# Kernel optimization log

Measured on AMD Instinct MI355X. Metric: run time of the kernel, lower is better.

The kernel has to match this reference:

```python
import jax, jax.numpy as jnp
import numpy as np

EPS = 1e-4  # performer softmax-kernel stabilizer
LN_EPS = 1e-5


def _layernorm(x, g, b):
    m = jnp.mean(x, axis=-1, keepdims=True)
    v = jnp.mean(jnp.square(x - m), axis=-1, keepdims=True)
    return (x - m) * jax.lax.rsqrt(v + LN_EPS) * g + b


def _softmax_features(x, proj, is_query):
    # FAVOR+ positive softmax-kernel features. x: [B,H,N,Dh], proj: [M,Dh]
    d = x.shape[-1]
    xn = x * (d ** -0.25)                      # data normalizer d^{-1/4}
    u = jnp.einsum('bhnd,md->bhnm', xn, proj)  # [B,H,N,M]
    diag = 0.5 * jnp.sum(jnp.square(xn), axis=-1, keepdims=True)
    if is_query:
        stab = jnp.max(u, axis=-1, keepdims=True)
    else:
        stab = jnp.max(u, axis=(-2, -1), keepdims=True)
    ratio = proj.shape[0] ** -0.5
    return ratio * (jnp.exp(u - diag - stab) + EPS)


def reference(x, proj, ln1_g, ln1_b, ln2_g, ln2_b, W1, b1, W2, b2):
    B, N, E = x.shape
    M, Dh = proj.shape
    H = E // Dh

    # --- multi-head fast attention sublayer (pre-LN, q=k=v, no dropout) ---
    h = _layernorm(x, ln1_g, ln1_b)
    qkv = h.reshape(B, N, H, Dh).transpose(0, 2, 1, 3)     # [B,H,N,Dh]
    q_p = _softmax_features(qkv, proj, is_query=True)      # [B,H,N,M]
    k_p = _softmax_features(qkv, proj, is_query=False)     # [B,H,N,M]

    # non-causal linear attention: O(N*M*Dh)
    k_sum = jnp.sum(k_p, axis=-2)                          # [B,H,M]
    d_inv = 1.0 / jnp.einsum('bhnm,bhm->bhn', q_p, k_sum)  # [B,H,N]
    ctx = jnp.einsum('bhnm,bhnd->bhmd', k_p, qkv)          # [B,H,M,Dh]
    attn = jnp.einsum('bhnm,bhmd,bhn->bhnd', q_p, ctx, d_inv)
    attn = attn.transpose(0, 2, 1, 3).reshape(B, N, E)
    x = x + attn

    # --- MLP sublayer (pre-LN, GELU, dropout off in eval) ---
    h2 = _layernorm(x, ln2_g, ln2_b)
    h2 = jax.nn.gelu(h2 @ W1 + b1, approximate=False) @ W2 + b2
    return x + h2


def setup_inputs() -> dict:
    B, N, E, H, M, F = 4, 2048, 768, 12, 256, 3072
    Dh = E // H
    key = jax.random.key(0)
    ks = jax.random.split(key, 4)
    return {
        'x': jax.random.normal(ks[0], (B, N, E), jnp.float32),
        'proj': jax.random.normal(ks[1], (M, Dh), jnp.float32),
        'ln1_g': jnp.ones((E,), jnp.float32),
        'ln1_b': jnp.zeros((E,), jnp.float32),
        'ln2_g': jnp.ones((E,), jnp.float32),
        'ln2_b': jnp.zeros((E,), jnp.float32),
        'W1': jax.random.normal(ks[2], (E, F), jnp.float32) * 0.02,
        'b1': jnp.zeros((F,), jnp.float32),
        'W2': jax.random.normal(ks[3], (F, E), jnp.float32) * 0.02,
        'b2': jnp.zeros((E,), jnp.float32),
    }
```

## Files before the change

kernel.cpp:

```cpp
#include <hip/hip_runtime.h>
#include <hip/hip_bf16.h>
#include <math.h>

#define B_    4
#define N_    2048
#define E_    768
#define H_    12
#define M_    256
#define F_    3072
#define DH_   64
#define BN_   (B_ * N_)
#define BH_   (B_ * H_)
#define NSP_  16

#define EPS_F     1e-4f
#define LN_EPS_F  1e-5f
#define DNORM_F   0.35355339059327373f
#define DIAGC_F   0.0625f

typedef __attribute__((ext_vector_type(8))) short bf16x8;
typedef __attribute__((ext_vector_type(4))) float f32x4;

static __device__ __forceinline__ float to_f32(float v) { return v; }
static __device__ __forceinline__ float to_f32(__hip_bfloat16 v) { return __bfloat162float(v); }
static __device__ __forceinline__ short f2bf(float v) {
    __hip_bfloat16 b = __float2bfloat16(v);
    return *reinterpret_cast<short*>(&b);
}

static __device__ __forceinline__ float fast_gelu(float x) {
    float xc = fminf(fmaxf(x, -9.f), 9.f);
    float y = 0.7978845608028654f * (xc + 0.044715f * xc * xc * xc);
    float tt = __expf(-2.f * y);
    return x * __builtin_amdgcn_rcpf(1.f + tt);
}

static __device__ __forceinline__ void gld_lds16(const void* g, void* lds) {
    __builtin_amdgcn_global_load_lds((const __attribute__((address_space(1))) void*)g,
                                     (__attribute__((address_space(3))) void*)lds, 16, 0, 0);
}

__global__ void probe_kernel(const unsigned int* __restrict__ g1, int* __restrict__ flag) {
    if (threadIdx.x == 0 && blockIdx.x == 0)
        *flag = (*g1 == 0x3F803F80u) ? 1 : 0;
}

__global__ void convert_kernel(const void* __restrict__ src, __hip_bfloat16* __restrict__ dst,
                               int n, const int* __restrict__ flag) {
    int isb = *flag;
    int i = blockIdx.x * blockDim.x + threadIdx.x;
    int stride = gridDim.x * blockDim.x;
    if (isb) {
        const unsigned short* s = (const unsigned short*)src;
        unsigned short* d = (unsigned short*)dst;
        for (; i < n; i += stride) d[i] = s[i];
    } else {
        const float* s = (const float*)src;
        for (; i < n; i += stride) dst[i] = __float2bfloat16(s[i]);
    }
}

__global__ void convert_transpose_kernel(const void* __restrict__ src,
                                         __hip_bfloat16* __restrict__ dst,
                                         int R, int C, const int* __restrict__ flag) {
    __shared__ __hip_bfloat16 tile[32][33];
    int isb = *flag;
    int c0 = blockIdx.x * 32, r0 = blockIdx.y * 32;
    int tx = threadIdx.x & 31, ty = threadIdx.x >> 5;
    if (isb) {
        const unsigned short* s = (const unsigned short*)src;
        for (int j = 0; j < 4; ++j) {
            int r = ty + j * 8;
            ((unsigned short*)&tile[r][tx])[0] = s[(size_t)(r0 + r) * C + c0 + tx];
        }
    } else {
        const float* s = (const float*)src;
        for (int j = 0; j < 4; ++j) {
            int r = ty + j * 8;
            tile[r][tx] = __float2bfloat16(s[(size_t)(r0 + r) * C + c0 + tx]);
        }
    }
    __syncthreads();
    for (int j = 0; j < 4; ++j) {
        int r = ty + j * 8;
        dst[(size_t)(c0 + r) * R + r0 + tx] = tile[tx][r];
    }
}

template <typename TIn>
__global__ void ln_kernel(const TIn* __restrict__ x,
                          const __hip_bfloat16* __restrict__ g,
                          const __hip_bfloat16* __restrict__ b,
                          __hip_bfloat16* __restrict__ hout,
                          float* __restrict__ diag ) {
    int row = blockIdx.x;
    int t = threadIdx.x;
    __shared__ float rs[256], rq[256];
    __shared__ float hrow[E_];

    float xv[3];
    const TIn* xr = x + (size_t)row * E_;
    float s = 0.f, q = 0.f;
    for (int i = 0; i < 3; ++i) {
        xv[i] = to_f32(xr[t + i * 256]);
        s += xv[i];
        q += xv[i] * xv[i];
    }
    rs[t] = s; rq[t] = q;
    __syncthreads();
    for (int off = 128; off > 0; off >>= 1) {
        if (t < off) { rs[t] += rs[t + off]; rq[t] += rq[t + off]; }
        __syncthreads();
    }
    float mean = rs[0] * (1.0f / E_);
    float var  = rq[0] * (1.0f / E_) - mean * mean;
    float rinv = rsqrtf(fmaxf(var, 0.0f) + LN_EPS_F);

    __hip_bfloat16* hr = hout + (size_t)row * E_;
    for (int i = 0; i < 3; ++i) {
        int e = t + i * 256;
        float hv = (xv[i] - mean) * rinv * __bfloat162float(g[e]) + __bfloat162float(b[e]);
        hr[e] = __float2bfloat16(hv);
        hrow[e] = hv;
    }
    if (diag != nullptr) {
        __syncthreads();
        if (t < H_) {
            float acc = 0.f;
            for (int k = 0; k < DH_; ++k) { float v = hrow[t * DH_ + k]; acc += v * v; }
            diag[row * H_ + t] = DIAGC_F * acc;
        }
    }
}

__global__ __launch_bounds__(256) void ctx_mfma_kernel(
        const __hip_bfloat16* __restrict__ h,
        const __hip_bfloat16* __restrict__ proj,
        const float* __restrict__ diag,
        float* __restrict__ pctx, float* __restrict__ pksum,
        float* __restrict__ pmax, float* __restrict__ pvsum) {
    int sp = blockIdx.x, bh = blockIdx.y;
    int bb = bh / H_, hh = bh % H_;
    int n0 = sp * 128;
    int t = threadIdx.x, lane = t & 63, w = t >> 6;
    int lm = lane & 15, kg = lane >> 4;

    __shared__ __align__(16) short hv_s[128 * 72];
    __shared__ __align__(16) short vt_s[64 * 136];
    __shared__ __align__(16) short p_s[64 * 72];
    __shared__ __align__(16) short kpt_s[64 * 136];
    __shared__ float ksp_s[4][64];
    __shared__ float dg_s[128];
    __shared__ float wmax_s[4];
    __shared__ float vp_s[4][64];

    for (int it = 0; it < 4; ++it) {
        int c = t + it * 256; int n = c >> 3, kb = c & 7;
        uint4 vld = *(const uint4*)&h[((size_t)(bb * N_ + n0 + n)) * E_ + hh * DH_ + kb * 8];
        *(uint4*)&hv_s[n * 72 + kb * 8] = vld;
        union { uint4 u4; short sh[8]; } uu; uu.u4 = vld;
        for (int j = 0; j < 8; ++j) vt_s[(kb * 8 + j) * 136 + n] = uu.sh[j];
    }
    if (t < 128) dg_s[t] = diag[(size_t)(bb * N_ + n0 + t) * H_ + hh];
    __syncthreads();

    {
        int d = t & 63, rg = t >> 6;
        float s = 0.f;
        for (int n = rg * 32; n < rg * 32 + 32; ++n)
            s += __bfloat162float(*(const __hip_bfloat16*)&hv_s[n * 72 + d]);
        vp_s[rg][d] = s;
    }
    __syncthreads();
    if (t < 64)
        pvsum[((size_t)sp * BH_ + bh) * 64 + t] =
            vp_s[0][t] + vp_s[1][t] + vp_s[2][t] + vp_s[3][t];

    for (int q = 0; q < 4; ++q) {
        __syncthreads();
        for (int it = 0; it < 2; ++it) {
            int c = t + it * 256; int m = c >> 3, kb = c & 7;
            *(uint4*)&p_s[m * 72 + kb * 8] = *(const uint4*)&proj[(size_t)(q * 64 + m) * DH_ + kb * 8];
        }
        __syncthreads();

        f32x4 u[2][4];
        for (int i = 0; i < 2; ++i) for (int j = 0; j < 4; ++j) u[i][j] = (f32x4){0.f,0.f,0.f,0.f};
        for (int kc = 0; kc < 2; ++kc) {
            bf16x8 af[2], bf[4];
            for (int i = 0; i < 2; ++i)
                af[i] = *(const bf16x8*)&hv_s[(w * 32 + i * 16 + lm) * 72 + kc * 32 + kg * 8];
            for (int j = 0; j < 4; ++j)
                bf[j] = *(const bf16x8*)&p_s[(j * 16 + lm) * 72 + kc * 32 + kg * 8];
            for (int i = 0; i < 2; ++i)
                for (int j = 0; j < 4; ++j)
                    u[i][j] = __builtin_amdgcn_mfma_f32_16x16x32_bf16(af[i], bf[j], u[i][j], 0, 0, 0);
        }
        float lmax = -1e30f;
        for (int i = 0; i < 2; ++i) for (int j = 0; j < 4; ++j) for (int r = 0; r < 4; ++r) {
            u[i][j][r] *= DNORM_F;
            lmax = fmaxf(lmax, u[i][j][r]);
        }
        for (int off = 32; off >= 1; off >>= 1) lmax = fmaxf(lmax, __shfl_xor(lmax, off));
        if (lane == 0) wmax_s[w] = lmax;
        __syncthreads();
        float Lmax = fmaxf(fmaxf(wmax_s[0], wmax_s[1]), fmaxf(wmax_s[2], wmax_s[3]));

        float kpart[4] = {0.f, 0.f, 0.f, 0.f};
        for (int i = 0; i < 2; ++i) {
            float dgv[4];
            for (int r = 0; r < 4; ++r) dgv[r] = dg_s[w * 32 + i * 16 + kg * 4 + r];
            for (int j = 0; j < 4; ++j)
                for (int r = 0; r < 4; ++r) {
                    float val = expf(u[i][j][r] - dgv[r] - Lmax);
                    kpart[j] += val;
                    kpt_s[(j * 16 + lm) * 136 + (w * 32 + i * 16 + kg * 4 + r)] = f2bf(val);
                }
        }
        for (int j = 0; j < 4; ++j) {
            kpart[j] += __shfl_xor(kpart[j], 16);
            kpart[j] += __shfl_xor(kpart[j], 32);
        }
        if (lane < 16)
            for (int j = 0; j < 4; ++j) ksp_s[w][j * 16 + lm] = kpart[j];
        __syncthreads();

        f32x4 c4[4];
        for (int jd = 0; jd < 4; ++jd) c4[jd] = (f32x4){0.f,0.f,0.f,0.f};
        for (int kc = 0; kc < 4; ++kc) {
            bf16x8 a = *(const bf16x8*)&kpt_s[(w * 16 + lm) * 136 + kc * 32 + kg * 8];
            for (int jd = 0; jd < 4; ++jd) {
                bf16x8 b = *(const bf16x8*)&vt_s[(jd * 16 + lm) * 136 + kc * 32 + kg * 8];
                c4[jd] = __builtin_amdgcn_mfma_f32_16x16x32_bf16(a, b, c4[jd], 0, 0, 0);
            }
        }
        size_t base = ((size_t)sp * BH_ + bh) * M_ + q * 64 + w * 16;
        for (int jd = 0; jd < 4; ++jd)
            for (int r = 0; r < 4; ++r)
                pctx[(base + kg * 4 + r) * DH_ + jd * 16 + lm] = c4[jd][r];
        if (t < 64)
            pksum[((size_t)sp * BH_ + bh) * M_ + q * 64 + t] =
                ksp_s[0][t] + ksp_s[1][t] + ksp_s[2][t] + ksp_s[3][t];
        if (t == 0) pmax[bh * 64 + sp * 4 + q] = Lmax;
    }
}

__global__ void ctx_reduce_kernel(const float* __restrict__ pctx,
                                  const float* __restrict__ pksum,
                                  const float* __restrict__ pmax,
                                  const float* __restrict__ pvsum,
                                  __hip_bfloat16* __restrict__ ctx_t,
                                  float* __restrict__ ksum) {
    int mb = blockIdx.x, bh = blockIdx.y;
    int t = threadIdx.x;
    __shared__ float hm_s;
    __shared__ float sc_s[16];
    __shared__ float vs_s[64];
    __shared__ float tr_s[64 * 65];
    if (t < 64) {
        float v = pmax[bh * 64 + t];
        for (int off = 32; off >= 1; off >>= 1) v = fmaxf(v, __shfl_xor(v, off));
        if (t == 0) hm_s = v;
        float s = 0.f;
        for (int sp = 0; sp < 16; ++sp) s += pvsum[((size_t)sp * BH_ + bh) * 64 + t];
        vs_s[t] = s;
    }
    __syncthreads();
    if (t < 16) sc_s[t] = expf(pmax[bh * 64 + t * 4 + mb] - hm_s);
    __syncthreads();
    float scl[16];
    for (int sp = 0; sp < 16; ++sp) scl[sp] = sc_s[sp];
    int d = t & 63;
    for (int it = 0; it < 16; ++it) {
        int ml = (t >> 6) + it * 4;
        float acc = 0.f;
        for (int sp = 0; sp < 16; ++sp)
            acc += scl[sp] * pctx[(((size_t)sp * BH_ + bh) * M_ + mb * 64 + ml) * DH_ + d];
        tr_s[ml * 65 + d] = acc + EPS_F * vs_s[d];
    }
    if (t < 64) {
        float ka = 0.f;
        for (int sp = 0; sp < 16; ++sp)
            ka += scl[sp] * pksum[((size_t)sp * BH_ + bh) * M_ + mb * 64 + t];
        ksum[bh * M_ + mb * 64 + t] = ka + EPS_F * (float)N_;
    }
    __syncthreads();
    int mcol = t & 63;
    for (int jt = 0; jt < 16; ++jt) {
        int dl = (t >> 6) + jt * 4;
        ctx_t[((size_t)bh * DH_ + dl) * M_ + mb * 64 + mcol] = __float2bfloat16(tr_s[mcol * 65 + dl]);
    }
}

__global__ void sums_kernel(const __hip_bfloat16* __restrict__ ctx_t,
                            const float* __restrict__ ksum,
                            float* __restrict__ ctxsum, float* __restrict__ kssum) {
    int bh = blockIdx.x, t = threadIdx.x;
    __shared__ float red[256];
    int d = t >> 2, part = t & 3;
    float s = 0.f;
    for (int mm = part * 64; mm < part * 64 + 64; ++mm)
        s += __bfloat162float(ctx_t[((size_t)bh * DH_ + d) * M_ + mm]);
    red[t] = s;
    __syncthreads();
    if (t < 64) ctxsum[bh * 64 + t] = red[t * 4] + red[t * 4 + 1] + red[t * 4 + 2] + red[t * 4 + 3];
    __syncthreads();
    red[t] = ksum[bh * M_ + t];
    __syncthreads();
    for (int off = 128; off > 0; off >>= 1) {
        if (t < off) red[t] += red[t + off];
        __syncthreads();
    }
    if (t == 0) kssum[bh] = red[0];
}

__global__ __launch_bounds__(256) void attn_mfma_kernel(
        const __hip_bfloat16* __restrict__ h,
        const __hip_bfloat16* __restrict__ proj,
        const float* __restrict__ diag,
        const __hip_bfloat16* __restrict__ ctx_t,
        const float* __restrict__ ksum,
        const float* __restrict__ ctxsum,
        const float* __restrict__ kssum,
        const __hip_bfloat16* __restrict__ xin,
        float* __restrict__ x2) {
    int ntile = blockIdx.x, bh = blockIdx.y;
    int bb = bh / H_, hh = bh % H_;
    int n0 = ntile * 128;
    int t = threadIdx.x, lane = t & 63, w = t >> 6;
    int lm = lane & 15, kg = lane >> 4;

    __shared__ __align__(16) short hq_s[128 * 72];
    __shared__ __align__(16) short p_s[64 * 72];
    __shared__ __align__(16) short ct_s[64 * 72];
    __shared__ __align__(16) short qp_s[128 * 72];
    __shared__ float ksum_s[256];
    __shared__ float dg_s[128];
    __shared__ float cs_s[64];
    __shared__ float kss_s;

    for (int it = 0; it < 4; ++it) {
        int c = t + it * 256; int n = c >> 3, kb = c & 7;
        *(uint4*)&hq_s[n * 72 + kb * 8] =
            *(const uint4*)&h[((size_t)(bb * N_ + n0 + n)) * E_ + hh * DH_ + kb * 8];
    }
    if (t < 128) dg_s[t] = diag[(size_t)(bb * N_ + n0 + t) * H_ + hh];
    ksum_s[t] = ksum[bh * M_ + t];
    if (t < 64) cs_s[t] = ctxsum[bh * 64 + t];
    if (t == 0) kss_s = kssum[bh];

    f32x4 o[2][4];
    float qs[2][4], mrun[2][4];
    for (int i = 0; i < 2; ++i)
        for (int jd = 0; jd < 4; ++jd) o[i][jd] = (f32x4){0.f,0.f,0.f,0.f};
    for (int i = 0; i < 2; ++i)
        for (int r = 0; r < 4; ++r) { qs[i][r] = 0.f; mrun[i][r] = -1e30f; }

    for (int mc = 0; mc < 4; ++mc) {
        __syncthreads();
        for (int it = 0; it < 2; ++it) {
            int c = t + it * 256; int m = c >> 3, kb = c & 7;
            *(uint4*)&p_s[m * 72 + kb * 8] = *(const uint4*)&proj[(size_t)(mc * 64 + m) * DH_ + kb * 8];
            *(uint4*)&ct_s[m * 72 + kb * 8] =
                *(const uint4*)&ctx_t[((size_t)bh * DH_ + m) * M_ + mc * 64 + kb * 8];
        }
        __syncthreads();

        f32x4 u[2][4];
        for (int i = 0; i < 2; ++i) for (int j = 0; j < 4; ++j) u[i][j] = (f32x4){0.f,0.f,0.f,0.f};
        for (int kc = 0; kc < 2; ++kc) {
            bf16x8 af[2], bf[4];
            for (int i = 0; i < 2; ++i)
                af[i] = *(const bf16x8*)&hq_s[(w * 32 + i * 16 + lm) * 72 + kc * 32 + kg * 8];
            for (int j = 0; j < 4; ++j)
                bf[j] = *(const bf16x8*)&p_s[(j * 16 + lm) * 72 + kc * 32 + kg * 8];
            for (int i = 0; i < 2; ++i)
                for (int j = 0; j < 4; ++j)
                    u[i][j] = __builtin_amdgcn_mfma_f32_16x16x32_bf16(af[i], bf[j], u[i][j], 0, 0, 0);
        }
        for (int i = 0; i < 2; ++i) for (int j = 0; j < 4; ++j)
            for (int r = 0; r < 4; ++r) u[i][j][r] *= DNORM_F;

        for (int i = 0; i < 2; ++i)
            for (int r = 0; r < 4; ++r) {
                float cm = fmaxf(fmaxf(u[i][0][r], u[i][1][r]), fmaxf(u[i][2][r], u[i][3][r]));
                for (int off = 8; off >= 1; off >>= 1) cm = fmaxf(cm, __shfl_xor(cm, off));
                float mnew = fmaxf(mrun[i][r], cm);
                float sc = expf(mrun[i][r] - mnew);
                mrun[i][r] = mnew;
                qs[i][r] *= sc;
                for (int jd = 0; jd < 4; ++jd) o[i][jd][r] *= sc;
            }
        for (int i = 0; i < 2; ++i) {
            float dgv[4];
            for (int r = 0; r < 4; ++r) dgv[r] = dg_s[w * 32 + i * 16 + kg * 4 + r];
            for (int j = 0; j < 4; ++j) {
                float ksv = ksum_s[mc * 64 + j * 16 + lm];
                for (int r = 0; r < 4; ++r) {
                    float val = expf(u[i][j][r] - dgv[r] - mrun[i][r]);
                    qs[i][r] += val * ksv;
                    qp_s[(w * 32 + i * 16 + kg * 4 + r) * 72 + j * 16 + lm] = f2bf(val);
                }
            }
        }
        __syncthreads();
        for (int kc = 0; kc < 2; ++kc) {
            bf16x8 af[2], bf[4];
            for (int i = 0; i < 2; ++i)
                af[i] = *(const bf16x8*)&qp_s[(w * 32 + i * 16 + lm) * 72 + kc * 32 + kg * 8];
            for (int jd = 0; jd < 4; ++jd)
                bf[jd] = *(const bf16x8*)&ct_s[(jd * 16 + lm) * 72 + kc * 32 + kg * 8];
            for (int i = 0; i < 2; ++i)
                for (int jd = 0; jd < 4; ++jd)
                    o[i][jd] = __builtin_amdgcn_mfma_f32_16x16x32_bf16(af[i], bf[jd], o[i][jd], 0, 0, 0);
        }
    }

    for (int i = 0; i < 2; ++i)
        for (int r = 0; r < 4; ++r)
            for (int off = 8; off >= 1; off >>= 1) qs[i][r] += __shfl_xor(qs[i][r], off);
    float kss = kss_s;
    for (int i = 0; i < 2; ++i)
        for (int r = 0; r < 4; ++r) {
            float dinv = 1.0f / (qs[i][r] + EPS_F * kss);
            size_t row = (size_t)(bb * N_ + n0 + w * 32 + i * 16 + kg * 4 + r);
            for (int jd = 0; jd < 4; ++jd) {
                int dcol = jd * 16 + lm;
                float outv = (o[i][jd][r] + EPS_F * cs_s[dcol]) * dinv;
                int col = hh * DH_ + dcol;
                x2[row * E_ + col] = __bfloat162float(xin[row * E_ + col]) + outv;
            }
        }
}

template <int KK, int NCOLS, int TM, bool DO_GELU>
__global__ __launch_bounds__(256) void mfma_mlp_kernel(
        const __hip_bfloat16* __restrict__ A,
        const __hip_bfloat16* __restrict__ Bt,
        const __hip_bfloat16* __restrict__ bias,
        const float* __restrict__ resid,
        void* __restrict__ outv,
        const int* __restrict__ oflag) {
    constexpr int TN = 128;
    constexpr int WR = TM / 64;
    constexpr int WC = 4 / WR;
    constexpr int PW = TN / WC;
    constexpr int NB = PW / 16;
    constexpr int CA = TM / 16;
    constexpr int CB = TN / 16;
    constexpr int CPS = CA + CB;
    constexpr int CPW = CPS / 4;
    constexpr int LBUF = CPS * 512;
    constexpr int NT = KK / 32;
    constexpr int NXB = NCOLS / TN;
    constexpr int NWG = NXB * (BN_ / TM);
    constexpr int CPX = NWG / 8;

    const int t = threadIdx.x;
    const int bid0 = blockIdx.y * NXB + blockIdx.x;
    const int bid = (bid0 & 7) * CPX + (bid0 >> 3);
    const int col0 = (bid % NXB) * TN;
    const int row0 = (bid / NXB) * TM;

    const int lane = t & 63, w = t >> 6;
    const int wr = w % WR, wc = w / WR;
    const int lm = lane & 15, kg = lane >> 4;
    const int lp = lane ^ ((lane >> 3) & 7);
    const int lr = lp >> 2, lc = (lp & 3) * 8;
    const int sxa = (lm >> 1) << 3;

    __shared__ __align__(16) short Ls[3 * LBUF];

    const __hip_bfloat16* gp[CPW];
    int lof[CPW];
#pragma unroll
    for (int cc = 0; cc < CPW; ++cc) {
        int c = w + cc * 4;
        gp[cc] = (c < CA) ? &A[(size_t)(row0 + c * 16 + lr) * KK + lc]
                          : &Bt[(size_t)(col0 + (c - CA) * 16 + lr) * KK + lc];
        lof[cc] = c * 512;
    }

    f32x4 acc[4][NB];
#pragma unroll
    for (int i = 0; i < 4; ++i)
#pragma unroll
        for (int j = 0; j < NB; ++j)
            acc[i][j] = (f32x4){0.f, 0.f, 0.f, 0.f};

#pragma unroll
    for (int cc = 0; cc < CPW; ++cc) gld_lds16(gp[cc], &Ls[lof[cc]]);
#pragma unroll
    for (int cc = 0; cc < CPW; ++cc) gld_lds16(gp[cc] + 32, &Ls[LBUF + lof[cc]]);

    int cur = 0;
    for (int ts = 0; ts < NT; ++ts) {
        if (ts + 2 < NT) {
            const int nb3 = (cur >= 1) ? (cur - 1) : 2;
            const int ko = (ts + 2) * 32;
#pragma unroll
            for (int cc = 0; cc < CPW; ++cc)
                gld_lds16(gp[cc] + ko, &Ls[nb3 * LBUF + lof[cc]]);
        }
        if (ts + 2 < NT)      asm volatile("s_waitcnt vmcnt(%0)" :: "n"(2 * CPW) : "memory");
        else if (ts + 1 < NT) asm volatile("s_waitcnt vmcnt(%0)" :: "n"(CPW) : "memory");
        else                  asm volatile("s_waitcnt vmcnt(0)" ::: "memory");
        __builtin_amdgcn_s_barrier();

        const short* base = &Ls[cur * LBUF];
        bf16x8 af[4], bfr[NB];
#pragma unroll
        for (int i = 0; i < 4; ++i)
            af[i] = *(const bf16x8*)&base[(((wr * 64 + i * 16 + lm) * 32) + kg * 8) ^ sxa];
#pragma unroll
        for (int j = 0; j < NB; ++j)
            bfr[j] = *(const bf16x8*)&base[(((CA * 16 + wc * PW + j * 16 + lm) * 32) + kg * 8) ^ sxa];

        asm volatile("s_waitcnt lgkmcnt(0)" ::: "memory");
        __builtin_amdgcn_sched_barrier(0);
        __builtin_amdgcn_s_barrier();

#pragma unroll
        for (int i = 0; i < 4; ++i)
#pragma unroll
            for (int j = 0; j < NB; ++j)
                acc[i][j] = __builtin_amdgcn_mfma_f32_16x16x32_bf16(af[i], bfr[j], acc[i][j], 0, 0, 0);
        cur = (cur == 2) ? 0 : (cur + 1);
    }

    int ob = DO_GELU ? 1 : *oflag;
#pragma unroll
    for (int i = 0; i < 4; ++i) {
#pragma unroll
        for (int r = 0; r < 4; ++r) {
            int row = row0 + wr * 64 + i * 16 + kg * 4 + r;
            size_t rb = (size_t)row * NCOLS;
#pragma unroll
            for (int j = 0; j < NB; ++j) {
                int col = col0 + wc * PW + j * 16 + lm;
                float v = acc[i][j][r] + __bfloat162float(bias[col]);
                if (DO_GELU) {
                    v = fast_gelu(v);
                } else {
                    v += resid[rb + col];
                }
                if (ob) ((__hip_bfloat16*)outv)[rb + col] = __float2bfloat16(v);
                else    ((float*)outv)[rb + col] = v;
            }
        }
    }
}

extern "C" void kernel_launch(void* const* d_in, const int* in_sizes, int n_in,
                              void* d_out, int out_size, void* d_ws, size_t ws_size,
                              hipStream_t stream) {
    char* ws = (char*)d_ws;
    size_t off = 0;
    auto carve = [&](size_t bytes) -> void* {
        void* p = ws + off;
        off += (bytes + 255) & ~(size_t)255;
        return p;
    };
    float*          x2    = (float*)carve((size_t)BN_ * E_ * 4);
    __hip_bfloat16* h     = (__hip_bfloat16*)carve((size_t)BN_ * E_ * 2);
    __hip_bfloat16* Wt1   = (__hip_bfloat16*)carve((size_t)E_ * F_ * 2);
    __hip_bfloat16* Wt2   = (__hip_bfloat16*)carve((size_t)F_ * E_ * 2);
    __hip_bfloat16* projc = (__hip_bfloat16*)carve((size_t)M_ * DH_ * 2);
    __hip_bfloat16* g1c   = (__hip_bfloat16*)carve((size_t)E_ * 2);
    __hip_bfloat16* b1lc  = (__hip_bfloat16*)carve((size_t)E_ * 2);
    __hip_bfloat16* g2c   = (__hip_bfloat16*)carve((size_t)E_ * 2);
    __hip_bfloat16* b2lc  = (__hip_bfloat16*)carve((size_t)E_ * 2);
    __hip_bfloat16* bb1c  = (__hip_bfloat16*)carve((size_t)F_ * 2);
    __hip_bfloat16* bb2c  = (__hip_bfloat16*)carve((size_t)E_ * 2);
    int*            flag  = (int*)carve(256);
    size_t mark = off;
    __hip_bfloat16* xc    = (__hip_bfloat16*)carve((size_t)BN_ * E_ * 2);
    float*          diag  = (float*)carve((size_t)BN_ * H_ * 4);
    float*          pctx  = (float*)carve((size_t)NSP_ * BH_ * M_ * DH_ * 4);
    float*          pksum = (float*)carve((size_t)NSP_ * BH_ * M_ * 4);
    float*          pmax  = (float*)carve((size_t)BH_ * 64 * 4);
    float*          pvsum = (float*)carve((size_t)NSP_ * BH_ * 64 * 4);
    __hip_bfloat16* ctx_t = (__hip_bfloat16*)carve((size_t)BH_ * DH_ * M_ * 2);
    float*          ksum  = (float*)carve((size_t)BH_ * M_ * 4);
    float*          ctxsum= (float*)carve((size_t)BH_ * DH_ * 4);
    float*          kssum = (float*)carve((size_t)BH_ * 4);
    __hip_bfloat16* h2    = h;
    __hip_bfloat16* mid   = (__hip_bfloat16*)(ws + mark);

    probe_kernel<<<1, 64, 0, stream>>>((const unsigned int*)d_in[2], flag);
    struct { const void* src; __hip_bfloat16* dst; int n; } cv[8] = {
        { d_in[0], xc,    BN_ * E_ },
        { d_in[1], projc, M_ * DH_ },
        { d_in[2], g1c,   E_ },
        { d_in[3], b1lc,  E_ },
        { d_in[4], g2c,   E_ },
        { d_in[5], b2lc,  E_ },
        { d_in[7], bb1c,  F_ },
        { d_in[9], bb2c,  E_ },
    };
    for (int i = 0; i < 8; ++i) {
        int blocks = (cv[i].n + 255) / 256; if (blocks > 1024) blocks = 1024;
        convert_kernel<<<blocks, 256, 0, stream>>>(cv[i].src, cv[i].dst, cv[i].n, flag);
    }
    convert_transpose_kernel<<<dim3(F_ / 32, E_ / 32), 256, 0, stream>>>(d_in[6], Wt1, E_, F_, flag);
    convert_transpose_kernel<<<dim3(E_ / 32, F_ / 32), 256, 0, stream>>>(d_in[8], Wt2, F_, E_, flag);

    ln_kernel<__hip_bfloat16><<<BN_, 256, 0, stream>>>(xc, g1c, b1lc, h, diag);
    ctx_mfma_kernel<<<dim3(NSP_, BH_), 256, 0, stream>>>(h, projc, diag, pctx, pksum, pmax, pvsum);
    ctx_reduce_kernel<<<dim3(4, BH_), 256, 0, stream>>>(pctx, pksum, pmax, pvsum, ctx_t, ksum);
    sums_kernel<<<BH_, 256, 0, stream>>>(ctx_t, ksum, ctxsum, kssum);
    attn_mfma_kernel<<<dim3(16, BH_), 256, 0, stream>>>(h, projc, diag, ctx_t, ksum, ctxsum, kssum, xc, x2);

    ln_kernel<float><<<BN_, 256, 0, stream>>>(x2, g2c, b2lc, h2, nullptr);
    mfma_mlp_kernel<E_, F_, 128, true><<<dim3(F_ / 128, BN_ / 128), 256, 0, stream>>>(
        h2, Wt1, bb1c, nullptr, (void*)mid, flag);
    mfma_mlp_kernel<F_, E_, 64, false><<<dim3(E_ / 128, BN_ / 64), 256, 0, stream>>>(
        mid, Wt2, bb2c, x2, d_out, flag);
}
```

Before: 388.3 us.

## Switch MLP GEMM to K=64 double-buffered steps with 128x128 tiles

Result: no change. 380.7 us (-2.0%).

```diff
diff --git a/kernel.cpp b/kernel.cpp
--- a/kernel.cpp
+++ b/kernel.cpp
@@ -433,25 +433,21 @@
         }
 }
 
-template <int KK, int NCOLS, int TM, bool DO_GELU>
-__global__ __launch_bounds__(256) void mfma_mlp_kernel(
+template <int KK, int NCOLS, bool DO_GELU>
+__global__ __launch_bounds__(256, 2) void mfma_mlp_kernel(
         const __hip_bfloat16* __restrict__ A,
         const __hip_bfloat16* __restrict__ Bt,
         const __hip_bfloat16* __restrict__ bias,
         const float* __restrict__ resid,
         void* __restrict__ outv,
         const int* __restrict__ oflag) {
-    constexpr int TN = 128;
-    constexpr int WR = TM / 64;
-    constexpr int WC = 4 / WR;
-    constexpr int PW = TN / WC;
-    constexpr int NB = PW / 16;
+    constexpr int TM = 128, TN = 128;
     constexpr int CA = TM / 16;
-    constexpr int CB = TN / 16;
-    constexpr int CPS = CA + CB;
+    constexpr int CPP = CA + TN / 16;
+    constexpr int CPS = 2 * CPP;
     constexpr int CPW = CPS / 4;
     constexpr int LBUF = CPS * 512;
-    constexpr int NT = KK / 32;
+    constexpr int NT = KK / 64;
     constexpr int NXB = NCOLS / TN;
     constexpr int NWG = NXB * (BN_ / TM);
     constexpr int CPX = NWG / 8;
@@ -463,69 +459,72 @@
     const int row0 = (bid / NXB) * TM;
 
     const int lane = t & 63, w = t >> 6;
-    const int wr = w % WR, wc = w / WR;
+    const int wr = w & 1, wc = w >> 1;
     const int lm = lane & 15, kg = lane >> 4;
     const int lp = lane ^ ((lane >> 3) & 7);
     const int lr = lp >> 2, lc = (lp & 3) * 8;
     const int sxa = (lm >> 1) << 3;
 
-    __shared__ __align__(16) short Ls[3 * LBUF];
+    __shared__ __align__(16) short Ls[2 * LBUF];
 
     const __hip_bfloat16* gp[CPW];
     int lof[CPW];
 #pragma unroll
     for (int cc = 0; cc < CPW; ++cc) {
         int c = w + cc * 4;
-        gp[cc] = (c < CA) ? &A[(size_t)(row0 + c * 16 + lr) * KK + lc]
-                          : &Bt[(size_t)(col0 + (c - CA) * 16 + lr) * KK + lc];
+        int p = c >> 4, tc = c & 15;
+        gp[cc] = (tc < CA) ? &A[(size_t)(row0 + tc * 16 + lr) * KK + p * 32 + lc]
+                           : &Bt[(size_t)(col0 + (tc - CA) * 16 + lr) * KK + p * 32 + lc];
         lof[cc] = c * 512;
     }
 
-    f32x4 acc[4][NB];
+    f32x4 acc[4][4];
 #pragma unroll
     for (int i = 0; i < 4; ++i)
 #pragma unroll
-        for (int j = 0; j < NB; ++j)
+        for (int j = 0; j < 4; ++j)
             acc[i][j] = (f32x4){0.f, 0.f, 0.f, 0.f};
 
 #pragma unroll
     for (int cc = 0; cc < CPW; ++cc) gld_lds16(gp[cc], &Ls[lof[cc]]);
-#pragma unroll
-    for (int cc = 0; cc < CPW; ++cc) gld_lds16(gp[cc] + 32, &Ls[LBUF + lof[cc]]);
 
     int cur = 0;
     for (int ts = 0; ts < NT; ++ts) {
-        if (ts + 2 < NT) {
-            const int nb3 = (cur >= 1) ? (cur - 1) : 2;
-            const int ko = (ts + 2) * 32;
+        if (ts + 1 < NT) {
+            const int nb = (cur ^ 1) * LBUF;
+            const int ko = (ts + 1) * 64;
 #pragma unroll
             for (int cc = 0; cc < CPW; ++cc)
-                gld_lds16(gp[cc] + ko, &Ls[nb3 * LBUF + lof[cc]]);
-        }
-        if (ts + 2 < NT)      asm volatile("s_waitcnt vmcnt(%0)" :: "n"(2 * CPW) : "memory");
-        else if (ts + 1 < NT) asm volatile("s_waitcnt vmcnt(%0)" :: "n"(CPW) : "memory");
-        else                  asm volatile("s_waitcnt vmcnt(0)" ::: "memory");
+                gld_lds16(gp[cc] + ko, &Ls[nb + lof[cc]]);
+            asm volatile("s_waitcnt vmcnt(%0)" :: "n"(CPW) : "memory");
+        } else {
+            asm volatile("s_waitcnt vmcnt(0)" ::: "memory");
+        }
         __builtin_amdgcn_s_barrier();
 
         const short* base = &Ls[cur * LBUF];
-        bf16x8 af[4], bfr[NB];
-#pragma unroll
-        for (int i = 0; i < 4; ++i)
-            af[i] = *(const bf16x8*)&base[(((wr * 64 + i * 16 + lm) * 32) + kg * 8) ^ sxa];
-#pragma unroll
-        for (int j = 0; j < NB; ++j)
-            bfr[j] = *(const bf16x8*)&base[(((CA * 16 + wc * PW + j * 16 + lm) * 32) + kg * 8) ^ sxa];
-
+        bf16x8 af[2][4], bfr[2][4];
+#pragma unroll
+        for (int p = 0; p < 2; ++p) {
+#pragma unroll
+            for (int i = 0; i < 4; ++i)
+                af[p][i] = *(const bf16x8*)&base[(p * CPP + wr * 4 + i) * 512 + ((lm * 32 + kg * 8) ^ sxa)];
+#pragma unroll
+            for (int j = 0; j < 4; ++j)
+                bfr[p][j] = *(const bf16x8*)&base[(p * CPP + CA + wc * 4 + j) * 512 + ((lm * 32 + kg * 8) ^ sxa)];
+        }
         asm volatile("s_waitcnt lgkmcnt(0)" ::: "memory");
         __builtin_amdgcn_sched_barrier(0);
         __builtin_amdgcn_s_barrier();
 
 #pragma unroll
-        for (int i = 0; i < 4; ++i)
-#pragma unroll
-            for (int j = 0; j < NB; ++j)
-                acc[i][j] = __builtin_amdgcn_mfma_f32_16x16x32_bf16(af[i], bfr[j], acc[i][j], 0, 0, 0);
-        cur = (cur == 2) ? 0 : (cur + 1);
+        for (int p = 0; p < 2; ++p)
+#pragma unroll
+            for (int i = 0; i < 4; ++i)
+#pragma unroll
+                for (int j = 0; j < 4; ++j)
+                    acc[i][j] = __builtin_amdgcn_mfma_f32_16x16x32_bf16(af[p][i], bfr[p][j], acc[i][j], 0, 0, 0);
+        cur ^= 1;
     }
 
     int ob = DO_GELU ? 1 : *oflag;
@@ -536,8 +535,8 @@
             int row = row0 + wr * 64 + i * 16 + kg * 4 + r;
             size_t rb = (size_t)row * NCOLS;
 #pragma unroll
-            for (int j = 0; j < NB; ++j) {
-                int col = col0 + wc * PW + j * 16 + lm;
+            for (int j = 0; j < 4; ++j) {
+                int col = col0 + wc * 64 + j * 16 + lm;
                 float v = acc[i][j][r] + __bfloat162float(bias[col]);
                 if (DO_GELU) {
                     v = fast_gelu(v);
@@ -612,8 +611,8 @@
     attn_mfma_kernel<<<dim3(16, BH_), 256, 0, stream>>>(h, projc, diag, ctx_t, ksum, ctxsum, kssum, xc, x2);
 
     ln_kernel<float><<<BN_, 256, 0, stream>>>(x2, g2c, b2lc, h2, nullptr);
-    mfma_mlp_kernel<E_, F_, 128, true><<<dim3(F_ / 128, BN_ / 128), 256, 0, stream>>>(
+    mfma_mlp_kernel<E_, F_, true><<<dim3(F_ / 128, BN_ / 128), 256, 0, stream>>>(
         h2, Wt1, bb1c, nullptr, (void*)mid, flag);
-    mfma_mlp_kernel<F_, E_, 64, false><<<dim3(E_ / 128, BN_ / 64), 256, 0, stream>>>(
+    mfma_mlp_kernel<F_, E_, false><<<dim3(E_ / 128, BN_ / 128), 256, 0, stream>>>(
         mid, Wt2, bb2c, x2, d_out, flag);
 }
```
